# Performance work log

Measured on AMD Instinct MI355X. Metric: run time of the kernel, lower is better.

The kernel has to match this reference:

```python
import jax, jax.numpy as jnp
import numpy as np

# Scalar quantization params (QLinear __init__ args)
FEATURE_BITWIDTH = 8
WEIGHT_BITWIDTH = 8
INPUT_ZERO_POINT = -3
OUTPUT_ZERO_POINT = -5
INPUT_SCALE = 0.05
OUTPUT_SCALE = 0.1
QMIN = -(1 << (FEATURE_BITWIDTH - 1))   # -128
QMAX = (1 << (FEATURE_BITWIDTH - 1)) - 1  # 127

M, K, N = 8192, 4096, 4096


def float_to_fixed_point(x, bitwidth):
    """Represent x (0 < x < 1) as int_scale * 2^-frac_bits with int_scale
    in [2^(bitwidth-2), 2^(bitwidth-1)) (mantissa fits in signed `bitwidth` bits)."""
    frac_bits = (bitwidth - 1 - jnp.ceil(jnp.log2(x))).astype(jnp.int32)
    int_scale = jnp.round(x * jnp.exp2(frac_bits.astype(jnp.float32))).astype(jnp.int32)
    return int_scale, frac_bits


def setup_inputs() -> dict:
    key = jax.random.key(0)
    k1, k2, k3, k4 = jax.random.split(key, 4)
    qinput = jax.random.randint(k1, (M, K), -128, 128, dtype=jnp.int8)
    qweight = jax.random.randint(k2, (N, K), -128, 128, dtype=jnp.int8)
    qbias = jax.random.randint(k3, (N,), -(1 << 16), 1 << 16, dtype=jnp.int32)
    # per-output-channel weight scale; keeps folded scale in (0, 1)
    weight_scale = jax.random.uniform(k4, (N,), jnp.float32, 0.002, 0.02)
    return {"qinput": qinput, "qweight": qweight, "qbias": qbias,
            "weight_scale": weight_scale}


def reference(qinput, qweight, qbias, weight_scale):
    w32 = qweight.astype(jnp.int32)                      # [N, K]
    # Qbias' = qbias - sum_k(qweight) * Zin  (bias shift folding input zero point)
    shifted_qbias = qbias - w32.sum(axis=1) * INPUT_ZERO_POINT  # [N]
    # int32 GEMM: [M, K] @ [K, N] + bias
    acc = qinput.astype(jnp.int32) @ w32.T + shifted_qbias[None, :]  # [M, N]
    # fixed-point requantization: (acc * int_scale) >> frac_bits + Zout
    folded_scale = INPUT_SCALE * weight_scale / OUTPUT_SCALE         # [N], in (0,1)
    int_scale, frac_bits = float_to_fixed_point(folded_scale, FEATURE_BITWIDTH)
    # widen to int64 for the multiply so the (acc * int_scale) product cannot wrap
    prod = acc.astype(jnp.int64) * int_scale.astype(jnp.int64)[None, :]
    scaled = jnp.right_shift(prod, frac_bits.astype(jnp.int64)[None, :])  # arithmetic >>
    out = scaled + OUTPUT_ZERO_POINT
    return jnp.clip(out, QMIN, QMAX).astype(jnp.int8)
```

## Files before the change

### kernel.cpp

```cpp
#include <hip/hip_runtime.h>
#include <cstdint>
#include <cstddef>

#define M_DIM 8192
#define N_DIM 4096
#define K_DIM 4096

#define BM 128
#define BN 128
#define BK 128

typedef int int32x4 __attribute__((ext_vector_type(4)));


typedef __attribute__((address_space(1))) const void* gas_cptr;
typedef __attribute__((address_space(3))) void* las_ptr;

__device__ __forceinline__ void async_copy16(const void* g, void* l) {
    __builtin_amdgcn_global_load_lds((gas_cptr)g, (las_ptr)l, 16, 0, 0);
}

__device__ __forceinline__ int32x4 pack16(const int* p) {
    const int32x4* v = (const int32x4*)p;
    int32x4 w0 = v[0], w1 = v[1], w2 = v[2], w3 = v[3];
    int32x4 r;
    r.x = (w0.x & 0xFF) | ((w0.y & 0xFF) << 8) | ((w0.z & 0xFF) << 16) | (w0.w << 24);
    r.y = (w1.x & 0xFF) | ((w1.y & 0xFF) << 8) | ((w1.z & 0xFF) << 16) | (w1.w << 24);
    r.z = (w2.x & 0xFF) | ((w2.y & 0xFF) << 8) | ((w2.z & 0xFF) << 16) | (w2.w << 24);
    r.w = (w3.x & 0xFF) | ((w3.y & 0xFF) << 8) | ((w3.z & 0xFF) << 16) | (w3.w << 24);
    return r;
}

__global__ void ql_detect_kernel(const int* a, const int* b, int* ws) {
    int t = threadIdx.x;
    int fa = 0, fb = 0;
    for (int i = t; i < 4096; i += 64) {
        int va = a[i]; if (va > 127 || va < -128) fa = 1;
        int vb = b[i]; if (vb > 127 || vb < -128) fb = 1;
    }
    unsigned long long ba = __ballot(fa);
    unsigned long long bb = __ballot(fb);
    if (t == 0) { ws[0] = ba ? 1 : 0; ws[1] = bb ? 1 : 0; }
}

__global__ __launch_bounds__(256)
void ql_pack_kernel(const void* src, int8_t* dst, const int* ws, int flag_idx, long n16) {
    const int f8 = __builtin_amdgcn_readfirstlane(ws[flag_idx]);
    long c = (long)blockIdx.x * 256 + threadIdx.x;
    if (c >= n16) return;
    if (f8) {
        ((int32x4*)dst)[c] = ((const int32x4*)src)[c];
    } else {
        ((int32x4*)dst)[c] = pack16((const int*)src + c * 16);
    }
}

__global__ void ql_prep_kernel(const void* wptr, const int* qbias,
                               const float* wscale, int* ws) {
    const int lane = threadIdx.x & 63;
    const int wid  = threadIdx.x >> 6;
    const int n = blockIdx.x * 4 + wid;
    const int b8 = __builtin_amdgcn_readfirstlane(ws[1]);

    int s = 0;
    if (b8) {
        const int32x4* row = (const int32x4*)((const int8_t*)wptr + (size_t)n * K_DIM);
        for (int c = lane; c < K_DIM / 16; c += 64) {
            int32x4 v = row[c];
#pragma unroll
            for (int j = 0; j < 4; ++j) {
                int w = (j == 0) ? v.x : (j == 1) ? v.y : (j == 2) ? v.z : v.w;
                s += (int)(int8_t)(w) + (int)(int8_t)(w >> 8)
                   + (int)(int8_t)(w >> 16) + (int)(int8_t)(w >> 24);
            }
        }
    } else {
        const int32x4* row = (const int32x4*)((const int*)wptr + (size_t)n * K_DIM);
        for (int c = lane; c < K_DIM / 4; c += 64) {
            int32x4 v = row[c];
            s += v.x + v.y + v.z + v.w;
        }
    }
#pragma unroll
    for (int off = 32; off > 0; off >>= 1) s += __shfl_down(s, off, 64);

    if (lane == 0) {
        ws[16 + n] = qbias[n] + 3 * s;
        float folded = (0.05f * wscale[n]) / 0.1f;
        int fbits = (int)(7.0f - ceilf(log2f(folded)));
        int isc = (int)rintf(folded * exp2f((float)fbits));
        ws[16 + N_DIM + n] = isc;
        ws[16 + 2 * N_DIM + n] = fbits;
    }
}

__device__ __forceinline__ void ql_epilogue(int32x4 acc[4][4], const int* ws,
                                            int* out, int bm, int bn,
                                            int wm, int wn, int qm, int qh) {
    const int* qb  = ws + 16;
    const int* isc = ws + 16 + N_DIM;
    const int* fbt = ws + 16 + 2 * N_DIM;
#pragma unroll
    for (int j = 0; j < 4; ++j) {
        const int n_g = bn * BN + wn + j * 16 + qm;
        const int b0 = qb[n_g];
        const int s0 = isc[n_g];
        const int f0 = fbt[n_g];
#pragma unroll
        for (int i = 0; i < 4; ++i) {
            const int m_base = bm * BM + wm + i * 16 + qh * 4;
#pragma unroll
            for (int r = 0; r < 4; ++r) {
                int v = ((r == 0) ? acc[i][j].x : (r == 1) ? acc[i][j].y
                        : (r == 2) ? acc[i][j].z : acc[i][j].w) + b0;
                long long p = (long long)v * (long long)s0;
                int o = (int)(p >> f0) - 5;
                o = o < -128 ? -128 : (o > 127 ? 127 : o);
                out[(size_t)(m_base + r) * N_DIM + n_g] = o;
            }
        }
    }
}

__global__ __launch_bounds__(256)
void ql_gemm_kernel(const int8_t* aptr, const int8_t* bptr, const int* ws, int* out) {
    __shared__ int32x4 Als[BM * BK / 16];
    __shared__ int32x4 Bls[BN * BK / 16];

    const int t    = threadIdx.x;
    const int lane = t & 63;
    const int wid  = t >> 6;
    const int bn = blockIdx.x;
    const int bm = blockIdx.y;

    const int wm = (wid >> 1) * 64;
    const int wn = (wid & 1) * 64;
    const int qm = lane & 15;
    const int qh = lane >> 4;

    int32x4 acc[4][4] = {};

    for (int kt = 0; kt < K_DIM / BK; ++kt) {
        __syncthreads();
        const int k0 = kt * BK;
#pragma unroll
        for (int r = 0; r < 4; ++r) {
            const int c    = r * 256 + t;
            const int row  = c >> 3;
            const int colg = (c & 7) ^ (row & 7);
            const size_t offA = (size_t)(bm * BM + row) * K_DIM + k0 + colg * 16;
            const size_t offB = (size_t)(bn * BN + row) * K_DIM + k0 + colg * 16;
            async_copy16(aptr + offA, &Als[c]);
            async_copy16(bptr + offB, &Bls[c]);
        }
        __syncthreads();

#pragma unroll
        for (int s = 0; s < 2; ++s) {
            const int colk = s * 4 + qh;
            int32x4 af[4], bf[4];
#pragma unroll
            for (int i = 0; i < 4; ++i) {
                const int ra = wm + i * 16 + qm;
                const int rb = wn + i * 16 + qm;
                af[i] = Als[ra * 8 + (colk ^ (ra & 7))];
                bf[i] = Bls[rb * 8 + (colk ^ (rb & 7))];
            }
#pragma unroll
            for (int i = 0; i < 4; ++i)
#pragma unroll
                for (int j = 0; j < 4; ++j)
                    acc[i][j] = __builtin_amdgcn_mfma_i32_16x16x64_i8(
                        af[i], bf[j], acc[i][j], 0, 0, 0);
        }
    }
    ql_epilogue(acc, ws, out, bm, bn, wm, wn, qm, qh);
}

__global__ __launch_bounds__(256)
void ql_gemm_fb_kernel(const void* aptr, const void* bptr, const int* ws, int* out) {
    __shared__ int32x4 Als[BM * BK / 16];
    __shared__ int32x4 Bls[BN * BK / 16];

    const int a8 = __builtin_amdgcn_readfirstlane(ws[0]);
    const int b8 = __builtin_amdgcn_readfirstlane(ws[1]);

    const int t    = threadIdx.x;
    const int lane = t & 63;
    const int wid  = t >> 6;
    const int bn = blockIdx.x;
    const int bm = blockIdx.y;

    const int wm = (wid >> 1) * 64;
    const int wn = (wid & 1) * 64;
    const int qm = lane & 15;
    const int qh = lane >> 4;

    int32x4 acc[4][4] = {};

    for (int kt = 0; kt < K_DIM / BK; ++kt) {
        __syncthreads();
        const int k0 = kt * BK;
#pragma unroll
        for (int r = 0; r < 4; ++r) {
            const int c    = r * 256 + t;
            const int row  = c >> 3;
            const int colg = (c & 7) ^ (row & 7);
            const size_t offA = (size_t)(bm * BM + row) * K_DIM + k0 + colg * 16;
            const size_t offB = (size_t)(bn * BN + row) * K_DIM + k0 + colg * 16;
            if (a8) async_copy16((const int8_t*)aptr + offA, &Als[c]);
            else    Als[c] = pack16((const int*)aptr + offA);
            if (b8) async_copy16((const int8_t*)bptr + offB, &Bls[c]);
            else    Bls[c] = pack16((const int*)bptr + offB);
        }
        __syncthreads();

#pragma unroll
        for (int s = 0; s < 2; ++s) {
            const int colk = s * 4 + qh;
            int32x4 af[4], bf[4];
#pragma unroll
            for (int i = 0; i < 4; ++i) {
                const int ra = wm + i * 16 + qm;
                const int rb = wn + i * 16 + qm;
                af[i] = Als[ra * 8 + (colk ^ (ra & 7))];
                bf[i] = Bls[rb * 8 + (colk ^ (rb & 7))];
            }
#pragma unroll
            for (int i = 0; i < 4; ++i)
#pragma unroll
                for (int j = 0; j < 4; ++j)
                    acc[i][j] = __builtin_amdgcn_mfma_i32_16x16x64_i8(
                        af[i], bf[j], acc[i][j], 0, 0, 0);
        }
    }
    ql_epilogue(acc, ws, out, bm, bn, wm, wn, qm, qh);
}

extern "C" void kernel_launch(void* const* d_in, const int* in_sizes, int n_in,
                              void* d_out, int out_size, void* d_ws, size_t ws_size,
                              hipStream_t stream) {
    const void* qin    = d_in[0];
    const void* qwt    = d_in[1];
    const int* qbias   = (const int*)d_in[2];
    const float* wscal = (const float*)d_in[3];
    int* ws  = (int*)d_ws;
    int* out = (int*)d_out;

    hipLaunchKernelGGL(ql_detect_kernel, dim3(1), dim3(64), 0, stream,
                       (const int*)qin, (const int*)qwt, ws);
    hipLaunchKernelGGL(ql_prep_kernel, dim3(N_DIM / 4), dim3(256), 0, stream,
                       qwt, qbias, wscal, ws);

    const size_t need = 65536 + (size_t)M_DIM * K_DIM + (size_t)N_DIM * K_DIM;
    if (ws_size >= need) {
        int8_t* a8 = (int8_t*)d_ws + 65536;
        int8_t* w8 = a8 + (size_t)M_DIM * K_DIM;
        const long nA = (long)M_DIM * K_DIM / 16;
        const long nW = (long)N_DIM * K_DIM / 16;
        hipLaunchKernelGGL(ql_pack_kernel, dim3((nA + 255) / 256), dim3(256), 0, stream,
                           qin, a8, ws, 0, nA);
        hipLaunchKernelGGL(ql_pack_kernel, dim3((nW + 255) / 256), dim3(256), 0, stream,
                           qwt, w8, ws, 1, nW);
        hipLaunchKernelGGL(ql_gemm_kernel, dim3(N_DIM / BN, M_DIM / BM), dim3(256), 0, stream,
                           a8, w8, ws, out);
    } else {
        hipLaunchKernelGGL(ql_gemm_fb_kernel, dim3(N_DIM / BN, M_DIM / BM), dim3(256), 0, stream,
                           qin, qwt, ws, out);
    }
}
```

Before: 443.9 us.

## Prepack operands into MFMA fragment order and load directly to registers

The pack kernels now reorder the int8 operands into per-128x128 tile blocks laid out exactly in MFMA fragment order. The GEMM kernel can then skip shared-memory staging and barriers, reading fragments straight from global memory into registers with a double-buffered prefetch. The epilogue stages each warp's outputs through shared memory so global stores are 16-byte vectorised rows instead of scattered scalar stores. The trade-off is a more complex pack pass and no cross-warp reuse of operand tiles through LDS, which raises global and L2 traffic.

```diff
diff --git a/kernel.cpp b/kernel.cpp
--- a/kernel.cpp
+++ b/kernel.cpp
@@ -44,14 +44,49 @@
 }
 
 __global__ __launch_bounds__(256)
-void ql_pack_kernel(const void* src, int8_t* dst, const int* ws, int flag_idx, long n16) {
+void ql_blockpack_kernel(const void* src, int8_t* dst, const int* ws, int flag_idx) {
+    __shared__ int lds[128 * 36];
     const int f8 = __builtin_amdgcn_readfirstlane(ws[flag_idx]);
-    long c = (long)blockIdx.x * 256 + threadIdx.x;
-    if (c >= n16) return;
+    const int kt = blockIdx.x;
+    const int rb = blockIdx.y;
+    const int t  = threadIdx.x;
+
     if (f8) {
-        ((int32x4*)dst)[c] = ((const int32x4*)src)[c];
+        const int r0 = t >> 3, c8 = t & 7;
+#pragma unroll
+        for (int it = 0; it < 4; ++it) {
+            const int row = r0 + it * 32;
+            int32x4 v = *(const int32x4*)((const int8_t*)src
+                         + (size_t)(rb * 128 + row) * K_DIM + kt * 128 + c8 * 16);
+            int* p = &lds[row * 36 + c8 * 4];
+            p[0] = v.x; p[1] = v.y; p[2] = v.z; p[3] = v.w;
+        }
     } else {
-        ((int32x4*)dst)[c] = pack16((const int*)src + c * 16);
+        const int r0 = t >> 5, c = t & 31;
+#pragma unroll
+        for (int it = 0; it < 16; ++it) {
+            const int row = r0 + it * 8;
+            const int* p = (const int*)src
+                         + (size_t)(rb * 128 + row) * K_DIM + kt * 128 + c * 4;
+            int32x4 v = *(const int32x4*)p;
+            lds[row * 36 + c] = (v.x & 0xFF) | ((v.y & 0xFF) << 8)
+                              | ((v.z & 0xFF) << 16) | (v.w << 24);
+        }
+    }
+    __syncthreads();
+
+    const size_t outBase = ((size_t)rb * gridDim.x + kt) * 16384;
+#pragma unroll
+    for (int rep = 0; rep < 4; ++rep) {
+        const int cI  = rep * 256 + t;
+        const int l   = cI & 63;
+        const int s   = (cI >> 6) & 1;
+        const int r16 = cI >> 7;
+        const int qm  = l & 15, qh = l >> 4;
+        const int ml  = r16 * 16 + qm;
+        const int kdw = s * 16 + qh * 4;
+        int32x4 v = *(const int32x4*)&lds[ml * 36 + kdw];
+        *(int32x4*)(dst + outBase + (size_t)cI * 16) = v;
     }
 }
 
@@ -71,7 +106,7 @@
             for (int j = 0; j < 4; ++j) {
                 int w = (j == 0) ? v.x : (j == 1) ? v.y : (j == 2) ? v.z : v.w;
                 s += (int)(int8_t)(w) + (int)(int8_t)(w >> 8)
-                   + (int)(int8_t)(w >> 16) + (int)(int8_t)(w >> 24);
+                   + (int)(int8_t)(w >> 16) + (w >> 24);
             }
         }
     } else {
@@ -94,38 +129,13 @@
     }
 }
 
-__device__ __forceinline__ void ql_epilogue(int32x4 acc[4][4], const int* ws,
-                                            int* out, int bm, int bn,
-                                            int wm, int wn, int qm, int qh) {
-    const int* qb  = ws + 16;
-    const int* isc = ws + 16 + N_DIM;
-    const int* fbt = ws + 16 + 2 * N_DIM;
-#pragma unroll
-    for (int j = 0; j < 4; ++j) {
-        const int n_g = bn * BN + wn + j * 16 + qm;
-        const int b0 = qb[n_g];
-        const int s0 = isc[n_g];
-        const int f0 = fbt[n_g];
-#pragma unroll
-        for (int i = 0; i < 4; ++i) {
-            const int m_base = bm * BM + wm + i * 16 + qh * 4;
-#pragma unroll
-            for (int r = 0; r < 4; ++r) {
-                int v = ((r == 0) ? acc[i][j].x : (r == 1) ? acc[i][j].y
-                        : (r == 2) ? acc[i][j].z : acc[i][j].w) + b0;
-                long long p = (long long)v * (long long)s0;
-                int o = (int)(p >> f0) - 5;
-                o = o < -128 ? -128 : (o > 127 ? 127 : o);
-                out[(size_t)(m_base + r) * N_DIM + n_g] = o;
-            }
-        }
-    }
+__device__ __forceinline__ int acc_elem(const int32x4& a, int r) {
+    return (r == 0) ? a.x : (r == 1) ? a.y : (r == 2) ? a.z : a.w;
 }
 
 __global__ __launch_bounds__(256)
-void ql_gemm_kernel(const int8_t* aptr, const int8_t* bptr, const int* ws, int* out) {
-    __shared__ int32x4 Als[BM * BK / 16];
-    __shared__ int32x4 Bls[BN * BK / 16];
+void ql_gemm_kernel(const int8_t* A8L, const int8_t* W8L, const int* ws, int* out) {
+    __shared__ int esc[4 * 16 * 68];
 
     const int t    = threadIdx.x;
     const int lane = t & 63;
@@ -138,43 +148,71 @@
     const int qm = lane & 15;
     const int qh = lane >> 4;
 
+    const int8_t* aW = A8L + (size_t)bm * (32 * 16384)
+                     + (size_t)((wid >> 1) * 4) * 2048 + lane * 16;
+    const int8_t* bW = W8L + (size_t)bn * (32 * 16384)
+                     + (size_t)((wid & 1) * 4) * 2048 + lane * 16;
+
     int32x4 acc[4][4] = {};
-
-    for (int kt = 0; kt < K_DIM / BK; ++kt) {
-        __syncthreads();
-        const int k0 = kt * BK;
-#pragma unroll
-        for (int r = 0; r < 4; ++r) {
-            const int c    = r * 256 + t;
-            const int row  = c >> 3;
-            const int colg = (c & 7) ^ (row & 7);
-            const size_t offA = (size_t)(bm * BM + row) * K_DIM + k0 + colg * 16;
-            const size_t offB = (size_t)(bn * BN + row) * K_DIM + k0 + colg * 16;
-            async_copy16(aptr + offA, &Als[c]);
-            async_copy16(bptr + offB, &Bls[c]);
-        }
-        __syncthreads();
-
-#pragma unroll
-        for (int s = 0; s < 2; ++s) {
-            const int colk = s * 4 + qh;
-            int32x4 af[4], bf[4];
+    int32x4 af[2][4], bf[2][4];
+
+#pragma unroll
+    for (int i = 0; i < 4; ++i) {
+        af[0][i] = *(const int32x4*)(aW + i * 2048);
+        bf[0][i] = *(const int32x4*)(bW + i * 2048);
+    }
+
+#pragma unroll 2
+    for (int st = 0; st < 64; ++st) {
+        const int cb = st & 1;
+        if (st < 63) {
+            const int nx = st + 1;
+            const size_t off = (size_t)(nx >> 1) * 16384 + (size_t)(nx & 1) * 1024;
 #pragma unroll
             for (int i = 0; i < 4; ++i) {
-                const int ra = wm + i * 16 + qm;
-                const int rb = wn + i * 16 + qm;
-                af[i] = Als[ra * 8 + (colk ^ (ra & 7))];
-                bf[i] = Bls[rb * 8 + (colk ^ (rb & 7))];
-            }
-#pragma unroll
-            for (int i = 0; i < 4; ++i)
-#pragma unroll
-                for (int j = 0; j < 4; ++j)
-                    acc[i][j] = __builtin_amdgcn_mfma_i32_16x16x64_i8(
-                        af[i], bf[j], acc[i][j], 0, 0, 0);
-        }
-    }
-    ql_epilogue(acc, ws, out, bm, bn, wm, wn, qm, qh);
+                af[cb ^ 1][i] = *(const int32x4*)(aW + off + i * 2048);
+                bf[cb ^ 1][i] = *(const int32x4*)(bW + off + i * 2048);
+            }
+        }
+#pragma unroll
+        for (int i = 0; i < 4; ++i)
+#pragma unroll
+            for (int j = 0; j < 4; ++j)
+                acc[i][j] = __builtin_amdgcn_mfma_i32_16x16x64_i8(
+                    af[cb][i], bf[cb][j], acc[i][j], 0, 0, 0);
+    }
+
+    const int* qb  = ws + 16;
+    const int* isc = ws + 16 + N_DIM;
+    const int* fbt = ws + 16 + 2 * N_DIM;
+    int* wsc = esc + wid * 1088;
+
+#pragma unroll
+    for (int i = 0; i < 4; ++i) {
+#pragma unroll
+        for (int j = 0; j < 4; ++j) {
+            const int n_g = bn * BN + wn + j * 16 + qm;
+            const int b0 = qb[n_g];
+            const int s0 = isc[n_g];
+            const int f0 = fbt[n_g];
+#pragma unroll
+            for (int r = 0; r < 4; ++r) {
+                int v = acc_elem(acc[i][j], r) + b0;
+                long long p = (long long)v * (long long)s0;
+                int o = (int)(p >> f0) - 5;
+                o = o < -128 ? -128 : (o > 127 ? 127 : o);
+                wsc[(qh * 4 + r) * 68 + j * 16 + qm] = o;
+            }
+        }
+#pragma unroll
+        for (int p4 = 0; p4 < 4; ++p4) {
+            const int lr = p4 * 4 + qh;
+            int32x4 vv = *(const int32x4*)&wsc[lr * 68 + qm * 4];
+            const size_t g = (size_t)(bm * BM + wm + i * 16 + lr) * N_DIM
+                           + bn * BN + wn + qm * 4;
+            *(int32x4*)(out + g) = vv;
+        }
+    }
 }
 
 __global__ __launch_bounds__(256)
@@ -234,7 +272,29 @@
                         af[i], bf[j], acc[i][j], 0, 0, 0);
         }
     }
-    ql_epilogue(acc, ws, out, bm, bn, wm, wn, qm, qh);
+
+    const int* qb  = ws + 16;
+    const int* isc = ws + 16 + N_DIM;
+    const int* fbt = ws + 16 + 2 * N_DIM;
+#pragma unroll
+    for (int j = 0; j < 4; ++j) {
+        const int n_g = bn * BN + wn + j * 16 + qm;
+        const int b0 = qb[n_g];
+        const int s0 = isc[n_g];
+        const int f0 = fbt[n_g];
+#pragma unroll
+        for (int i = 0; i < 4; ++i) {
+            const int m_base = bm * BM + wm + i * 16 + qh * 4;
+#pragma unroll
+            for (int r = 0; r < 4; ++r) {
+                int v = acc_elem(acc[i][j], r) + b0;
+                long long p = (long long)v * (long long)s0;
+                int o = (int)(p >> f0) - 5;
+                o = o < -128 ? -128 : (o > 127 ? 127 : o);
+                out[(size_t)(m_base + r) * N_DIM + n_g] = o;
+            }
+        }
+    }
 }
 
 extern "C" void kernel_launch(void* const* d_in, const int* in_sizes, int n_in,
@@ -254,16 +314,14 @@
 
     const size_t need = 65536 + (size_t)M_DIM * K_DIM + (size_t)N_DIM * K_DIM;
     if (ws_size >= need) {
-        int8_t* a8 = (int8_t*)d_ws + 65536;
-        int8_t* w8 = a8 + (size_t)M_DIM * K_DIM;
-        const long nA = (long)M_DIM * K_DIM / 16;
-        const long nW = (long)N_DIM * K_DIM / 16;
-        hipLaunchKernelGGL(ql_pack_kernel, dim3((nA + 255) / 256), dim3(256), 0, stream,
-                           qin, a8, ws, 0, nA);
-        hipLaunchKernelGGL(ql_pack_kernel, dim3((nW + 255) / 256), dim3(256), 0, stream,
-                           qwt, w8, ws, 1, nW);
+        int8_t* a8l = (int8_t*)d_ws + 65536;
+        int8_t* w8l = a8l + (size_t)M_DIM * K_DIM;
+        hipLaunchKernelGGL(ql_blockpack_kernel, dim3(K_DIM / 128, M_DIM / 128), dim3(256),
+                           0, stream, qin, a8l, ws, 0);
+        hipLaunchKernelGGL(ql_blockpack_kernel, dim3(K_DIM / 128, N_DIM / 128), dim3(256),
+                           0, stream, qwt, w8l, ws, 1);
         hipLaunchKernelGGL(ql_gemm_kernel, dim3(N_DIM / BN, M_DIM / BM), dim3(256), 0, stream,
-                           a8, w8, ws, out);
+                           a8l, w8l, ws, out);
     } else {
         hipLaunchKernelGGL(ql_gemm_fb_kernel, dim3(N_DIM / BN, M_DIM / BM), dim3(256), 0, stream,
                            qin, qwt, ws, out);
```

Result: slower. 747.5 us (+68.4%).

## Fuse weight row-sum into pack kernel, compute requant params in epilogue, swap grid order

Applied to the files above, without the earlier changes.

Merges the weight packing, the weight row-sum and the activation packing into one kernel launch, so the weight matrix is read once instead of twice and two launches go away. Bias folding and the fixed-point scale computation move into the GEMM epilogue, which now recomputes them per column from qbias and weight_scale. The GEMM grid is transposed so blockIdx.x walks M, which changes L2 reuse of the tiles. The epilogue gains some transcendental math per column, which is small next to the GEMM.

```diff
diff --git a/kernel.cpp b/kernel.cpp
--- a/kernel.cpp
+++ b/kernel.cpp
@@ -44,75 +44,83 @@
 }
 
 __global__ __launch_bounds__(256)
-void ql_pack_kernel(const void* src, int8_t* dst, const int* ws, int flag_idx, long n16) {
-    const int f8 = __builtin_amdgcn_readfirstlane(ws[flag_idx]);
-    long c = (long)blockIdx.x * 256 + threadIdx.x;
-    if (c >= n16) return;
-    if (f8) {
-        ((int32x4*)dst)[c] = ((const int32x4*)src)[c];
+void ql_pack_all_kernel(const void* asrc, const void* bsrc, int* adst, int* bdst,
+                        int* ws) {
+    const int fa = __builtin_amdgcn_readfirstlane(ws[0]);
+    const int fb = __builtin_amdgcn_readfirstlane(ws[1]);
+    const int t    = threadIdx.x;
+    const int lane = t & 63;
+    const int wid  = t >> 6;
+
+    if (blockIdx.x < N_DIM / 4) {
+        const int n = blockIdx.x * 4 + wid;
+        int s = 0;
+        if (fb) {
+            const int* src = (const int*)bsrc + (size_t)n * (K_DIM / 4);
+#pragma unroll
+            for (int it = 0; it < 4; ++it) {
+                const int c = it * 64 + lane;
+                int w = src[c];
+                bdst[(size_t)n * (K_DIM / 4) + c] = w;
+                s += (int)(int8_t)(w) + (int)(int8_t)(w >> 8)
+                   + (int)(int8_t)(w >> 16) + (w >> 24);
+            }
+        } else {
+            const int32x4* src = (const int32x4*)bsrc + (size_t)n * (K_DIM / 4);
+#pragma unroll
+            for (int it = 0; it < 16; ++it) {
+                const int c = it * 64 + lane;
+                int32x4 v = src[c];
+                int w = (v.x & 0xFF) | ((v.y & 0xFF) << 8)
+                      | ((v.z & 0xFF) << 16) | (v.w << 24);
+                bdst[(size_t)n * (K_DIM / 4) + c] = w;
+                s += v.x + v.y + v.z + v.w;
+            }
+        }
+#pragma unroll
+        for (int off = 32; off > 0; off >>= 1) s += __shfl_down(s, off, 64);
+        if (lane == 0) ws[16 + n] = s;
     } else {
-        ((int32x4*)dst)[c] = pack16((const int*)src + c * 16);
-    }
-}
-
-__global__ void ql_prep_kernel(const void* wptr, const int* qbias,
-                               const float* wscale, int* ws) {
-    const int lane = threadIdx.x & 63;
-    const int wid  = threadIdx.x >> 6;
-    const int n = blockIdx.x * 4 + wid;
-    const int b8 = __builtin_amdgcn_readfirstlane(ws[1]);
-
-    int s = 0;
-    if (b8) {
-        const int32x4* row = (const int32x4*)((const int8_t*)wptr + (size_t)n * K_DIM);
-        for (int c = lane; c < K_DIM / 16; c += 64) {
-            int32x4 v = row[c];
-#pragma unroll
-            for (int j = 0; j < 4; ++j) {
-                int w = (j == 0) ? v.x : (j == 1) ? v.y : (j == 2) ? v.z : v.w;
-                s += (int)(int8_t)(w) + (int)(int8_t)(w >> 8)
-                   + (int)(int8_t)(w >> 16) + (int)(int8_t)(w >> 24);
-            }
-        }
-    } else {
-        const int32x4* row = (const int32x4*)((const int*)wptr + (size_t)n * K_DIM);
-        for (int c = lane; c < K_DIM / 4; c += 64) {
-            int32x4 v = row[c];
-            s += v.x + v.y + v.z + v.w;
-        }
-    }
-#pragma unroll
-    for (int off = 32; off > 0; off >>= 1) s += __shfl_down(s, off, 64);
-
-    if (lane == 0) {
-        ws[16 + n] = qbias[n] + 3 * s;
-        float folded = (0.05f * wscale[n]) / 0.1f;
-        int fbits = (int)(7.0f - ceilf(log2f(folded)));
-        int isc = (int)rintf(folded * exp2f((float)fbits));
-        ws[16 + N_DIM + n] = isc;
-        ws[16 + 2 * N_DIM + n] = fbits;
-    }
-}
-
-__device__ __forceinline__ void ql_epilogue(int32x4 acc[4][4], const int* ws,
+        const long base = (long)(blockIdx.x - N_DIM / 4) * 1024;
+        if (fa) {
+#pragma unroll
+            for (int it = 0; it < 4; ++it) {
+                const long c = base + it * 256 + t;
+                adst[c] = ((const int*)asrc)[c];
+            }
+        } else {
+#pragma unroll
+            for (int it = 0; it < 4; ++it) {
+                const long c = base + it * 256 + t;
+                int32x4 v = ((const int32x4*)asrc)[c];
+                adst[c] = (v.x & 0xFF) | ((v.y & 0xFF) << 8)
+                        | ((v.z & 0xFF) << 16) | (v.w << 24);
+            }
+        }
+    }
+}
+
+__device__ __forceinline__ int acc_elem(const int32x4& a, int r) {
+    return (r == 0) ? a.x : (r == 1) ? a.y : (r == 2) ? a.z : a.w;
+}
+
+__device__ __forceinline__ void ql_epilogue(int32x4 acc[4][4], const int* rs,
+                                            const int* qbias, const float* wscale,
                                             int* out, int bm, int bn,
                                             int wm, int wn, int qm, int qh) {
-    const int* qb  = ws + 16;
-    const int* isc = ws + 16 + N_DIM;
-    const int* fbt = ws + 16 + 2 * N_DIM;
 #pragma unroll
     for (int j = 0; j < 4; ++j) {
         const int n_g = bn * BN + wn + j * 16 + qm;
-        const int b0 = qb[n_g];
-        const int s0 = isc[n_g];
-        const int f0 = fbt[n_g];
+        const int b0 = qbias[n_g] + 3 * rs[n_g];
+        float folded = (0.05f * wscale[n_g]) / 0.1f;
+        const int f0 = (int)(7.0f - ceilf(log2f(folded)));
+        const int s0 = (int)rintf(folded * exp2f((float)f0));
 #pragma unroll
         for (int i = 0; i < 4; ++i) {
             const int m_base = bm * BM + wm + i * 16 + qh * 4;
 #pragma unroll
             for (int r = 0; r < 4; ++r) {
-                int v = ((r == 0) ? acc[i][j].x : (r == 1) ? acc[i][j].y
-                        : (r == 2) ? acc[i][j].z : acc[i][j].w) + b0;
+                int v = acc_elem(acc[i][j], r) + b0;
                 long long p = (long long)v * (long long)s0;
                 int o = (int)(p >> f0) - 5;
                 o = o < -128 ? -128 : (o > 127 ? 127 : o);
@@ -123,15 +131,16 @@
 }
 
 __global__ __launch_bounds__(256)
-void ql_gemm_kernel(const int8_t* aptr, const int8_t* bptr, const int* ws, int* out) {
+void ql_gemm_kernel(const int8_t* aptr, const int8_t* bptr, const int* ws,
+                    const int* qbias, const float* wscale, int* out) {
     __shared__ int32x4 Als[BM * BK / 16];
     __shared__ int32x4 Bls[BN * BK / 16];
 
     const int t    = threadIdx.x;
     const int lane = t & 63;
     const int wid  = t >> 6;
-    const int bn = blockIdx.x;
-    const int bm = blockIdx.y;
+    const int bm = blockIdx.x;
+    const int bn = blockIdx.y;
 
     const int wm = (wid >> 1) * 64;
     const int wn = (wid & 1) * 64;
@@ -174,11 +183,42 @@
                         af[i], bf[j], acc[i][j], 0, 0, 0);
         }
     }
-    ql_epilogue(acc, ws, out, bm, bn, wm, wn, qm, qh);
+    ql_epilogue(acc, ws + 16, qbias, wscale, out, bm, bn, wm, wn, qm, qh);
+}
+
+__global__ void ql_prep_kernel(const void* wptr, int* ws) {
+    const int lane = threadIdx.x & 63;
+    const int wid  = threadIdx.x >> 6;
+    const int n = blockIdx.x * 4 + wid;
+    const int b8 = __builtin_amdgcn_readfirstlane(ws[1]);
+
+    int s = 0;
+    if (b8) {
+        const int32x4* row = (const int32x4*)((const int8_t*)wptr + (size_t)n * K_DIM);
+        for (int c = lane; c < K_DIM / 16; c += 64) {
+            int32x4 v = row[c];
+#pragma unroll
+            for (int j = 0; j < 4; ++j) {
+                int w = (j == 0) ? v.x : (j == 1) ? v.y : (j == 2) ? v.z : v.w;
+                s += (int)(int8_t)(w) + (int)(int8_t)(w >> 8)
+                   + (int)(int8_t)(w >> 16) + (w >> 24);
+            }
+        }
+    } else {
+        const int32x4* row = (const int32x4*)((const int*)wptr + (size_t)n * K_DIM);
+        for (int c = lane; c < K_DIM / 4; c += 64) {
+            int32x4 v = row[c];
+            s += v.x + v.y + v.z + v.w;
+        }
+    }
+#pragma unroll
+    for (int off = 32; off > 0; off >>= 1) s += __shfl_down(s, off, 64);
+    if (lane == 0) ws[16 + n] = s;
 }
 
 __global__ __launch_bounds__(256)
-void ql_gemm_fb_kernel(const void* aptr, const void* bptr, const int* ws, int* out) {
+void ql_gemm_fb_kernel(const void* aptr, const void* bptr, const int* ws,
+                       const int* qbias, const float* wscale, int* out) {
     __shared__ int32x4 Als[BM * BK / 16];
     __shared__ int32x4 Bls[BN * BK / 16];
 
@@ -188,8 +228,8 @@
     const int t    = threadIdx.x;
     const int lane = t & 63;
     const int wid  = t >> 6;
-    const int bn = blockIdx.x;
-    const int bm = blockIdx.y;
+    const int bm = blockIdx.x;
+    const int bn = blockIdx.y;
 
     const int wm = (wid >> 1) * 64;
     const int wn = (wid & 1) * 64;
@@ -234,7 +274,7 @@
                         af[i], bf[j], acc[i][j], 0, 0, 0);
         }
     }
-    ql_epilogue(acc, ws, out, bm, bn, wm, wn, qm, qh);
+    ql_epilogue(acc, ws + 16, qbias, wscale, out, bm, bn, wm, wn, qm, qh);
 }
 
 extern "C" void kernel_launch(void* const* d_in, const int* in_sizes, int n_in,
@@ -249,23 +289,20 @@
 
     hipLaunchKernelGGL(ql_detect_kernel, dim3(1), dim3(64), 0, stream,
                        (const int*)qin, (const int*)qwt, ws);
-    hipLaunchKernelGGL(ql_prep_kernel, dim3(N_DIM / 4), dim3(256), 0, stream,
-                       qwt, qbias, wscal, ws);
 
     const size_t need = 65536 + (size_t)M_DIM * K_DIM + (size_t)N_DIM * K_DIM;
     if (ws_size >= need) {
         int8_t* a8 = (int8_t*)d_ws + 65536;
         int8_t* w8 = a8 + (size_t)M_DIM * K_DIM;
-        const long nA = (long)M_DIM * K_DIM / 16;
-        const long nW = (long)N_DIM * K_DIM / 16;
-        hipLaunchKernelGGL(ql_pack_kernel, dim3((nA + 255) / 256), dim3(256), 0, stream,
-                           qin, a8, ws, 0, nA);
-        hipLaunchKernelGGL(ql_pack_kernel, dim3((nW + 255) / 256), dim3(256), 0, stream,
-                           qwt, w8, ws, 1, nW);
-        hipLaunchKernelGGL(ql_gemm_kernel, dim3(N_DIM / BN, M_DIM / BM), dim3(256), 0, stream,
-                           a8, w8, ws, out);
+        const unsigned packGrid = N_DIM / 4 + (unsigned)((size_t)M_DIM * K_DIM / 4096);
+        hipLaunchKernelGGL(ql_pack_all_kernel, dim3(packGrid), dim3(256), 0, stream,
+                           qin, qwt, (int*)a8, (int*)w8, ws);
+        hipLaunchKernelGGL(ql_gemm_kernel, dim3(M_DIM / BM, N_DIM / BN), dim3(256),
+                           0, stream, a8, w8, ws, qbias, wscal, out);
     } else {
-        hipLaunchKernelGGL(ql_gemm_fb_kernel, dim3(N_DIM / BN, M_DIM / BM), dim3(256), 0, stream,
-                           qin, qwt, ws, out);
-    }
-}
+        hipLaunchKernelGGL(ql_prep_kernel, dim3(N_DIM / 4), dim3(256), 0, stream,
+                           qwt, ws);
+        hipLaunchKernelGGL(ql_gemm_fb_kernel, dim3(M_DIM / BM, N_DIM / BN), dim3(256),
+                           0, stream, qin, qwt, ws, qbias, wscal, out);
+    }
+}
```

Result: slower. 475.4 us (+7.1%).
